# Optimization experiments

Hardware: AMD Instinct MI355X
Metric: run time of the kernel (lower is better)

## Reference

```python
import jax, jax.numpy as jnp
import numpy as np

B = 16384
D_VIS, D_LANG, D_STATE = 768, 768, 64
D = 256          # d_model
E = 4            # n_experts
K = 2            # top_k
D_IN = D_VIS + D_LANG + D_STATE
EPS = 1e-5


def layernorm(x, g, b):
    mu = x.mean(-1, keepdims=True)
    var = ((x - mu) ** 2).mean(-1, keepdims=True)
    return g * (x - mu) / jnp.sqrt(var + EPS) + b


def setup_inputs() -> dict:
    key = jax.random.key(0)
    ks = jax.random.split(key, 16)
    s = 0.02
    return {
        "vis": jax.random.normal(ks[0], (B, D_VIS), jnp.float32),
        "lang": jax.random.normal(ks[1], (B, D_LANG), jnp.float32),
        "state": jax.random.normal(ks[2], (B, D_STATE), jnp.float32),
        # fusion: Linear(d_in, d_model) + LayerNorm
        "Wf": jax.random.normal(ks[3], (D_IN, D), jnp.float32) * s,
        "bf": jnp.zeros((D,), jnp.float32),
        "gf": jnp.ones((D,), jnp.float32),
        "bfln": jnp.zeros((D,), jnp.float32),
        # gate (bias=False); random instead of zeros so routing is nontrivial
        "Wg": jax.random.normal(ks[4], (D, E), jnp.float32) * s,
        # stacked experts: Linear(d,2d) -> GELU -> Linear(2d,d) -> GELU -> Linear(d,d), then LN(x + net(x))
        "W1": jax.random.normal(ks[5], (E, D, 2 * D), jnp.float32) * s,
        "b1": jnp.zeros((E, 2 * D), jnp.float32),
        "W2": jax.random.normal(ks[6], (E, 2 * D, D), jnp.float32) * s,
        "b2": jnp.zeros((E, D), jnp.float32),
        "W3": jax.random.normal(ks[7], (E, D, D), jnp.float32) * s,
        "b3": jnp.zeros((E, D), jnp.float32),
        "eg": jnp.ones((E, D), jnp.float32),
        "eb": jnp.zeros((E, D), jnp.float32),
    }


def reference(vis, lang, state, Wf, bf, gf, bfln, Wg, W1, b1, W2, b2, W3, b3, eg, eb):
    gelu = lambda t: jax.nn.gelu(t, approximate=False)
    # fusion: Linear -> LayerNorm -> GELU  (dropout is eval-mode identity)
    x = jnp.concatenate([vis, lang, state], axis=-1) @ Wf + bf   # [B, D]
    x = gelu(layernorm(x, gf, bfln))

    logits = x @ Wg                                              # [B, E]
    all_probs = jax.nn.softmax(logits, axis=-1)
    top_vals, top_idx = jax.lax.top_k(logits, K)                 # [B, K]
    top_w = jax.nn.softmax(top_vals, axis=-1)                    # [B, K]

    # all experts densely (E small); original computes same math per masked subset
    h = gelu(jnp.einsum('bd,edh->beh', x, W1) + b1)              # [B, E, 2D]
    h = gelu(jnp.einsum('beh,ehd->bed', h, W2) + b2)             # [B, E, D]
    h = jnp.einsum('bed,edf->bef', h, W3) + b3                   # [B, E, D]
    y = layernorm(x[:, None, :] + h, eg, eb)                     # [B, E, D]

    # gather selected experts and combine with top-k weights
    y_sel = jnp.take_along_axis(y, top_idx[:, :, None], axis=1)  # [B, K, D]
    out = jnp.einsum('bk,bkd->bd', top_w, y_sel)                 # [B, D]

    # load-balance loss: importance x load
    counts = jnp.zeros((E,), x.dtype).at[top_idx.reshape(-1)].add(1.0)
    f_i = counts / (B * K)
    lb_loss = E * jnp.sum(f_i * all_probs.mean(0))
    return out, lb_loss
```

## Files before the change

kernel.cpp:

```cpp
#include <hip/hip_runtime.h>
#include <math.h>


typedef unsigned short u16;
typedef unsigned int u32;
typedef __attribute__((ext_vector_type(8))) short bf16x8;
typedef __attribute__((ext_vector_type(4))) float f32x4;

__device__ __forceinline__ float bf2f(u16 u) {
    union { u32 i; float f; } v; v.i = ((u32)u) << 16; return v.f;
}
__device__ __forceinline__ u16 f2bf(float f) {
    union { float f; u32 i; } v; v.f = f;
    u32 x = v.i;
    return (u16)((x + 0x7fffu + ((x >> 16) & 1u)) >> 16);
}
__device__ __forceinline__ float gelu_exact(float v) {
    return 0.5f * v * (1.0f + erff(v * 0.70710678118654752f));
}

typedef __attribute__((address_space(1))) void GV;
typedef __attribute__((address_space(3))) void SV;
__device__ __forceinline__ void gldlds(const void* g, void* l) {
    __builtin_amdgcn_global_load_lds((GV*)g, (SV*)l, 16, 0, 0);
}

__device__ __forceinline__ u32 pk2(u32 f0, u32 f1) {
    return __builtin_amdgcn_perm(f1, f0, 0x07060302);
}

__device__ __forceinline__ void stageA64(const u16* Ag, int lda, u16* As, int tid) {
#pragma unroll
    for (int i = 0; i < 2; ++i) {
        int s = i * 256 + tid;
        int m = s >> 3, c = s & 7;
        gldlds(Ag + m * lda + (c ^ (m & 7)) * 8, As + s * 8);
    }
}
__device__ __forceinline__ void stageB64(const u16* Bg, int ldb, u16* Bs, int tid) {
#pragma unroll
    for (int i = 0; i < 8; ++i) {
        int s = i * 256 + tid;
        int n = s >> 3, c = s & 7;
        gldlds(Bg + n * ldb + (c ^ (n & 7)) * 8, Bs + s * 8);
    }
}
__device__ __forceinline__ void compute64(const u16* As, const u16* Bs, f32x4 acc[4][4],
                                          int w, int l16, int quad) {
#pragma unroll
    for (int ks = 0; ks < 2; ++ks) {
        bf16x8 a[4];
#pragma unroll
        for (int mt = 0; mt < 4; ++mt) {
            int m = mt * 16 + l16;
            a[mt] = *(const bf16x8*)(As + m * 64 + (((ks * 4 + quad) ^ (m & 7)) << 3));
        }
#pragma unroll
        for (int nt = 0; nt < 4; ++nt) {
            int n = w * 64 + nt * 16 + l16;
            bf16x8 b = *(const bf16x8*)(Bs + n * 64 + (((ks * 4 + quad) ^ (n & 7)) << 3));
#pragma unroll
            for (int mt = 0; mt < 4; ++mt)
                acc[mt][nt] = __builtin_amdgcn_mfma_f32_16x16x32_bf16(a[mt], b, acc[mt][nt], 0, 0, 0);
        }
    }
}
__device__ __forceinline__ void stageA128_512(const u16* Ag, int lda, u16* As, int tid) {
#pragma unroll
    for (int i = 0; i < 2; ++i) {
        int s = i * 512 + tid;
        int m = s >> 3, c = s & 7;
        gldlds(Ag + m * lda + (c ^ (m & 7)) * 8, As + s * 8);
    }
}
__device__ __forceinline__ void stageB64_512(const u16* Bg, int ldb, u16* Bs, int tid) {
#pragma unroll
    for (int i = 0; i < 4; ++i) {
        int s = i * 512 + tid;
        int n = s >> 3, c = s & 7;
        gldlds(Bg + n * ldb + (c ^ (n & 7)) * 8, Bs + s * 8);
    }
}
__device__ __forceinline__ void compute128_8w(const u16* As, const u16* Bs, f32x4 acc[4][4],
                                              int wrw, int wc, int l16, int quad) {
#pragma unroll
    for (int ks = 0; ks < 2; ++ks) {
        bf16x8 a[4];
#pragma unroll
        for (int mt = 0; mt < 4; ++mt) {
            int m = wrw * 64 + mt * 16 + l16;
            a[mt] = *(const bf16x8*)(As + m * 64 + (((ks * 4 + quad) ^ (m & 7)) << 3));
        }
#pragma unroll
        for (int nt = 0; nt < 4; ++nt) {
            int n = wc * 64 + nt * 16 + l16;
            bf16x8 b = *(const bf16x8*)(Bs + n * 64 + (((ks * 4 + quad) ^ (n & 7)) << 3));
#pragma unroll
            for (int mt = 0; mt < 4; ++mt)
                acc[mt][nt] = __builtin_amdgcn_mfma_f32_16x16x32_bf16(a[mt], b, acc[mt][nt], 0, 0, 0);
        }
    }
}

__global__ __launch_bounds__(256) void prep_kernel(
    const float* __restrict__ Wf, const float* __restrict__ W1, const float* __restrict__ W2,
    const float* __restrict__ W3,
    u16* __restrict__ wft, u16* __restrict__ w1t, u16* __restrict__ w2t, u16* __restrict__ w3t,
    float* __restrict__ lbacc) {
    int b = blockIdx.x;
    int tid = threadIdx.x;
    const float* src; u16* dst; int K, N, kt, ntl;
    if (b < 400)      { src = Wf; dst = wft; K = 1600; N = 256; kt = b % 50; ntl = b / 50; }
    else if (b < 912) { int r = b - 400, e = r >> 7; r &= 127;
                        src = W1 + (size_t)e * 131072; dst = w1t + (size_t)e * 131072;
                        K = 256; N = 512; kt = r & 7; ntl = r >> 3; }
    else if (b < 1424){ int r = b - 912, e = r >> 7; r &= 127;
                        src = W2 + (size_t)e * 131072; dst = w2t + (size_t)e * 131072;
                        K = 512; N = 256; kt = r & 15; ntl = r >> 4; }
    else if (b < 1680){ int r = b - 1424, e = r >> 6; r &= 63;
                        src = W3 + (size_t)e * 65536; dst = w3t + (size_t)e * 65536;
                        K = 256; N = 256; kt = r & 7; ntl = r >> 3; }
    else { if (tid < 8) lbacc[tid] = 0.0f; return; }
    int k0 = kt * 32, n0 = ntl * 32;
    __shared__ float tl[32][33];
    int j = tid & 31, i0 = (tid >> 5) << 2;
#pragma unroll
    for (int ii = 0; ii < 4; ++ii)
        tl[i0 + ii][j] = src[(size_t)(k0 + i0 + ii) * N + n0 + j];
    __syncthreads();
#pragma unroll
    for (int ii = 0; ii < 4; ++ii)
        dst[(size_t)(n0 + i0 + ii) * K + k0 + j] = f2bf(tl[j][i0 + ii]);
}

__global__ __launch_bounds__(512, 4) void fusion_kernel(
    const float* __restrict__ vis, const float* __restrict__ lang, const float* __restrict__ state,
    const u16* __restrict__ BT, const float* __restrict__ bfv_, const float* __restrict__ gf,
    const float* __restrict__ bfln, const float* __restrict__ Wg,
    u16* __restrict__ xbf, float* __restrict__ wr, float* __restrict__ lbacc) {
    __shared__ __align__(16) u32 Af[2048];
    __shared__ __align__(16) u16 Bs[16384];
    int tid = threadIdx.x;
    int w = tid >> 6, lane = tid & 63, quad = lane >> 4, l16 = lane & 15;
    int m0 = blockIdx.x * 32;
    f32x4 acc[2][2] = {};

    for (int kit = 0; kit < 25; ++kit) {
        const float* base; int ld;
        if (kit < 12)      { base = vis   + (size_t)m0 * 768 + kit * 64;        ld = 768; }
        else if (kit < 24) { base = lang  + (size_t)m0 * 768 + (kit - 12) * 64; ld = 768; }
        else               { base = state + (size_t)m0 * 64;                    ld = 64; }
        {
            int s = tid;
            int m = s >> 4, c = s & 15;
            gldlds(base + m * ld + (c ^ (m & 15)) * 4, Af + s * 4);
        }
        stageB64_512(BT + kit * 64, 1600, Bs, tid);
        __syncthreads();
#pragma unroll
        for (int ks = 0; ks < 2; ++ks) {
            bf16x8 a[2];
#pragma unroll
            for (int mt = 0; mt < 2; ++mt) {
                int m = mt * 16 + l16;
                int c0 = ks * 8 + quad * 2;
                const u32* rowp = Af + m * 64;
                uint4 f0 = *(const uint4*)(rowp + (c0 ^ (m & 15)) * 4);
                uint4 f1 = *(const uint4*)(rowp + ((c0 + 1) ^ (m & 15)) * 4);
                union { u32 u[4]; bf16x8 v; } pk;
                pk.u[0] = pk2(f0.x, f0.y); pk.u[1] = pk2(f0.z, f0.w);
                pk.u[2] = pk2(f1.x, f1.y); pk.u[3] = pk2(f1.z, f1.w);
                a[mt] = pk.v;
            }
#pragma unroll
            for (int nt = 0; nt < 2; ++nt) {
                int n = w * 32 + nt * 16 + l16;
                bf16x8 b = *(const bf16x8*)(Bs + n * 64 + (((ks * 4 + quad) ^ (n & 7)) << 3));
#pragma unroll
                for (int mt = 0; mt < 2; ++mt)
                    acc[mt][nt] = __builtin_amdgcn_mfma_f32_16x16x32_bf16(a[mt], b, acc[mt][nt], 0, 0, 0);
            }
        }
        __syncthreads();
    }

    float2* red  = (float2*)Af;
    float*  muv  = (float*)(Af + 512);
    float*  rsv  = (float*)(Af + 544);
    float*  gred = (float*)(Af + 576);
    float*  sacc = (float*)(Af + 1600);

    float bv[2], gvv[2], blv[2]; float4 wgv[2];
#pragma unroll
    for (int nt = 0; nt < 2; ++nt) {
        int col = w * 32 + nt * 16 + l16;
        bv[nt] = bfv_[col]; gvv[nt] = gf[col]; blv[nt] = bfln[col];
        wgv[nt] = *(const float4*)(Wg + col * 4);
    }
    if (tid < 8) sacc[tid] = 0.f;
#pragma unroll
    for (int mt = 0; mt < 2; ++mt)
#pragma unroll
        for (int r = 0; r < 4; ++r) {
            float ss = 0.f, qq = 0.f;
#pragma unroll
            for (int nt = 0; nt < 2; ++nt) {
                float v = acc[mt][nt][r] + bv[nt];
                acc[mt][nt][r] = v;
                ss += v; qq += v * v;
            }
#pragma unroll
            for (int d = 1; d < 16; d <<= 1) { ss += __shfl_xor(ss, d); qq += __shfl_xor(qq, d); }
            if (l16 == 0) red[w * 32 + mt * 16 + quad * 4 + r] = make_float2(ss, qq);
        }
    __syncthreads();
    if (tid < 32) {
        float ss = 0.f, qq = 0.f;
#pragma unroll
        for (int ww = 0; ww < 8; ++ww) { float2 t = red[ww * 32 + tid]; ss += t.x; qq += t.y; }
        float mu = ss * (1.f / 256.f);
        float var = qq * (1.f / 256.f) - mu * mu;
        muv[tid] = mu;
        rsv[tid] = 1.f / sqrtf(var + 1e-5f);
    }
    __syncthreads();
#pragma unroll
    for (int mt = 0; mt < 2; ++mt)
#pragma unroll
        for (int r = 0; r < 4; ++r) {
            int rl = mt * 16 + quad * 4 + r;
            float mu = muv[rl], rs = rsv[rl];
#pragma unroll
            for (int nt = 0; nt < 2; ++nt) {
                int col = w * 32 + nt * 16 + l16;
                float t = (acc[mt][nt][r] - mu) * rs * gvv[nt] + blv[nt];
                float g = gelu_exact(t);
                acc[mt][nt][r] = g;
                xbf[(size_t)(m0 + rl) * 256 + col] = f2bf(g);
            }
        }
#pragma unroll
    for (int mt = 0; mt < 2; ++mt)
#pragma unroll
        for (int r = 0; r < 4; ++r) {
            int rl = mt * 16 + quad * 4 + r;
            float p0 = 0.f, p1 = 0.f, p2 = 0.f, p3 = 0.f;
#pragma unroll
            for (int nt = 0; nt < 2; ++nt) {
                float g = acc[mt][nt][r];
                p0 += g * wgv[nt].x; p1 += g * wgv[nt].y;
                p2 += g * wgv[nt].z; p3 += g * wgv[nt].w;
            }
#pragma unroll
            for (int d = 1; d < 16; d <<= 1) {
                p0 += __shfl_xor(p0, d); p1 += __shfl_xor(p1, d);
                p2 += __shfl_xor(p2, d); p3 += __shfl_xor(p3, d);
            }
            if (l16 == 0) {
                float* gp = gred + w * 128 + rl * 4;
                gp[0] = p0; gp[1] = p1; gp[2] = p2; gp[3] = p3;
            }
        }
    __syncthreads();
    if (tid < 32) {
        int row = tid;
        float lg[4];
#pragma unroll
        for (int e = 0; e < 4; ++e) {
            float s = 0.f;
#pragma unroll
            for (int ww = 0; ww < 8; ++ww) s += gred[ww * 128 + row * 4 + e];
            lg[e] = s;
        }
        float mx = fmaxf(fmaxf(lg[0], lg[1]), fmaxf(lg[2], lg[3]));
        float ex[4]; float Z = 0.f;
#pragma unroll
        for (int e = 0; e < 4; ++e) { ex[e] = expf(lg[e] - mx); Z += ex[e]; }
        int i0 = 0; float v0 = lg[0];
#pragma unroll
        for (int e = 1; e < 4; ++e) if (lg[e] > v0) { v0 = lg[e]; i0 = e; }
        int i1 = -1; float v1 = -1e30f;
#pragma unroll
        for (int e = 0; e < 4; ++e) if (e != i0 && lg[e] > v1) { v1 = lg[e]; i1 = e; }
        float t = expf(v1 - v0);
        float wA = 1.f / (1.f + t), wB = t / (1.f + t);
        float w4[4] = {0.f, 0.f, 0.f, 0.f};
        w4[i0] = wA; w4[i1] = wB;
#pragma unroll
        for (int e = 0; e < 4; ++e) wr[(size_t)(m0 + row) * 4 + e] = w4[e];
#pragma unroll
        for (int e = 0; e < 4; ++e) atomicAdd(&sacc[e], ex[e] / Z);
        atomicAdd(&sacc[4 + i0], 1.f);
        atomicAdd(&sacc[4 + i1], 1.f);
    }
    __syncthreads();
    if (tid < 8) atomicAdd(lbacc + tid, sacc[tid]);
}

__global__ __launch_bounds__(512, 4) void expert_gemm_kernel(
    const u16* __restrict__ A, int lda, size_t aE,
    const u16* __restrict__ BT, size_t bE,
    const float* __restrict__ bias, int biasE,
    u16* __restrict__ outp, int ldo, size_t oE) {
    __shared__ __align__(16) u16 As[8192];
    __shared__ __align__(16) u16 Bs[16384];
    int tid = threadIdx.x;
    int w = tid >> 6, lane = tid & 63, quad = lane >> 4, l16 = lane & 15;
    int wrw = w >> 2, wc = w & 3;
    int m0 = blockIdx.x * 128;
    int col0 = blockIdx.y * 256;
    int e = blockIdx.z;
    f32x4 acc[4][4] = {};
    const u16* Ag = A + e * aE + (size_t)m0 * lda;
    const u16* Bg = BT + e * bE + (size_t)col0 * lda;
    int kiters = lda >> 6;
    for (int kit = 0; kit < kiters; ++kit) {
        stageA128_512(Ag + kit * 64, lda, As, tid);
        stageB64_512(Bg + kit * 64, lda, Bs, tid);
        __syncthreads();
        compute128_8w(As, Bs, acc, wrw, wc, l16, quad);
        __syncthreads();
    }
#pragma unroll
    for (int nt = 0; nt < 4; ++nt) {
        int col = col0 + wc * 64 + nt * 16 + l16;
        float bvv = bias[e * biasE + col];
#pragma unroll
        for (int mt = 0; mt < 4; ++mt)
#pragma unroll
            for (int r = 0; r < 4; ++r) {
                int row = m0 + wrw * 64 + mt * 16 + quad * 4 + r;
                outp[e * oE + (size_t)row * ldo + col] = f2bf(gelu_exact(acc[mt][nt][r] + bvv));
            }
    }
}

__global__ __launch_bounds__(256) void combine_kernel(
    const u16* __restrict__ h2, const u16* __restrict__ W3T,
    const float* __restrict__ b3, const float* __restrict__ eg, const float* __restrict__ eb,
    const u16* __restrict__ xbf, const float* __restrict__ wr,
    const float* __restrict__ lbacc, float* __restrict__ outp) {
    __shared__ __align__(16) u16 As[4096];
    __shared__ __align__(16) u16 Bs[16384];
    __shared__ __align__(16) u16 xs[16384];
    __shared__ float wl[256];
    __shared__ float2 red[256];
    __shared__ float muv[64], rsv[64];
    int tid = threadIdx.x;
    int w = tid >> 6, lane = tid & 63, quad = lane >> 4, l16 = lane & 15;
    int m0 = blockIdx.x * 64;
    if (blockIdx.x == 0 && tid == 0) {
        float lb = 0.f;
#pragma unroll
        for (int e = 0; e < 4; ++e)
            lb += (lbacc[4 + e] / 32768.f) * (lbacc[e] / 16384.f);
        outp[4194304] = 4.f * lb;
    }
#pragma unroll
    for (int i = 0; i < 8; ++i) {
        int s = i * 256 + tid;
        *(uint4*)(xs + s * 8) = *(const uint4*)(xbf + (size_t)m0 * 256 + s * 8);
    }
    wl[tid] = wr[(size_t)m0 * 4 + tid];
    f32x4 oacc[4][4] = {};
    for (int e = 0; e < 4; ++e) {
        __syncthreads();
        f32x4 acc[4][4] = {};
        const u16* Ag = h2 + ((size_t)e * 16384 + m0) * 256;
        const u16* Bg = W3T + (size_t)e * 65536;
        for (int kit = 0; kit < 4; ++kit) {
            stageA64(Ag + kit * 64, 256, As, tid);
            stageB64(Bg + kit * 64, 256, Bs, tid);
            __syncthreads();
            compute64(As, Bs, acc, w, l16, quad);
            __syncthreads();
        }
        float b3v[4], egv[4], ebv[4];
#pragma unroll
        for (int nt = 0; nt < 4; ++nt) {
            int col = w * 64 + nt * 16 + l16;
            b3v[nt] = b3[e * 256 + col]; egv[nt] = eg[e * 256 + col]; ebv[nt] = eb[e * 256 + col];
        }
#pragma unroll
        for (int mt = 0; mt < 4; ++mt)
#pragma unroll
            for (int r = 0; r < 4; ++r) {
                int row = mt * 16 + quad * 4 + r;
                float ss = 0.f, qq = 0.f;
#pragma unroll
                for (int nt = 0; nt < 4; ++nt) {
                    int col = w * 64 + nt * 16 + l16;
                    float v = acc[mt][nt][r] + b3v[nt] + bf2f(xs[row * 256 + col]);
                    acc[mt][nt][r] = v;
                    ss += v; qq += v * v;
                }
#pragma unroll
                for (int d = 1; d < 16; d <<= 1) { ss += __shfl_xor(ss, d); qq += __shfl_xor(qq, d); }
                if (l16 == 0) red[w * 64 + row] = make_float2(ss, qq);
            }
        __syncthreads();
        if (tid < 64) {
            float ss = 0.f, qq = 0.f;
#pragma unroll
            for (int ww = 0; ww < 4; ++ww) { float2 t = red[ww * 64 + tid]; ss += t.x; qq += t.y; }
            float mu = ss * (1.f / 256.f);
            float var = qq * (1.f / 256.f) - mu * mu;
            muv[tid] = mu;
            rsv[tid] = 1.f / sqrtf(var + 1e-5f);
        }
        __syncthreads();
#pragma unroll
        for (int mt = 0; mt < 4; ++mt)
#pragma unroll
            for (int r = 0; r < 4; ++r) {
                int row = mt * 16 + quad * 4 + r;
                float mu = muv[row], rs = rsv[row], we = wl[row * 4 + e];
#pragma unroll
                for (int nt = 0; nt < 4; ++nt) {
                    float y = (acc[mt][nt][r] - mu) * rs * egv[nt] + ebv[nt];
                    oacc[mt][nt][r] += we * y;
                }
            }
    }
#pragma unroll
    for (int mt = 0; mt < 4; ++mt)
#pragma unroll
        for (int r = 0; r < 4; ++r) {
            int row = mt * 16 + quad * 4 + r;
#pragma unroll
            for (int nt = 0; nt < 4; ++nt) {
                int col = w * 64 + nt * 16 + l16;
                outp[(size_t)(m0 + row) * 256 + col] = oacc[mt][nt][r];
            }
        }
}

extern "C" void kernel_launch(void* const* d_in, const int* in_sizes, int n_in,
                              void* d_out, int out_size, void* d_ws, size_t ws_size,
                              hipStream_t stream) {
    const float* vis   = (const float*)d_in[0];
    const float* lang  = (const float*)d_in[1];
    const float* state = (const float*)d_in[2];
    const float* Wf    = (const float*)d_in[3];
    const float* bf_   = (const float*)d_in[4];
    const float* gf    = (const float*)d_in[5];
    const float* bfln  = (const float*)d_in[6];
    const float* Wg    = (const float*)d_in[7];
    const float* W1    = (const float*)d_in[8];
    const float* b1    = (const float*)d_in[9];
    const float* W2    = (const float*)d_in[10];
    const float* b2    = (const float*)d_in[11];
    const float* W3    = (const float*)d_in[12];
    const float* b3    = (const float*)d_in[13];
    const float* eg    = (const float*)d_in[14];
    const float* eb    = (const float*)d_in[15];
    float* outp = (float*)d_out;

    char* ws = (char*)d_ws;
    size_t off = 0;
    float* lbacc = (float*)(ws + off); off += 256;
    u16* WFT  = (u16*)(ws + off); off += 819200UL;
    u16* W1T  = (u16*)(ws + off); off += 1048576UL;
    u16* W2T  = (u16*)(ws + off); off += 1048576UL;
    u16* W3T  = (u16*)(ws + off); off += 524288UL;
    u16* XBF  = (u16*)(ws + off); off += 8388608UL;
    float* WR = (float*)(ws + off); off += 262144UL;
    u16* H1   = (u16*)(ws + off); off += 67108864UL;
    u16* H2   = (u16*)(ws + off); off += 33554432UL;
    if (ws_size < off) return;

    prep_kernel<<<1681, 256, 0, stream>>>(Wf, W1, W2, W3, WFT, W1T, W2T, W3T, lbacc);
    fusion_kernel<<<512, 512, 0, stream>>>(vis, lang, state, WFT, bf_, gf, bfln, Wg,
                                           XBF, WR, lbacc);
    expert_gemm_kernel<<<dim3(128, 2, 4), 512, 0, stream>>>(
        XBF, 256, 0, W1T, 131072, b1, 512, H1, 512, 8388608UL);
    expert_gemm_kernel<<<dim3(128, 1, 4), 512, 0, stream>>>(
        H1, 512, 8388608UL, W2T, 131072, b2, 256, H2, 256, 4194304UL);
    combine_kernel<<<256, 256, 0, stream>>>(H2, W3T, b3, eg, eb, XBF, WR, lbacc, outp);
}
```

Measured before the change: 319.6 us.

## Split combine per expert with atomics, stage expert GEMM stores, overlap weight prep

Three separate changes. The combine kernel is split across experts on a second grid dimension, and each block atomically adds its weighted LayerNorm output into a zero-initialised output. This quadruples the parallelism at the cost of a memset and float atomics, and the atomics make the order of summation nondeterministic. The expert GEMM epilogue now stages bf16 results through LDS with a swizzle so they can be written with coalesced 16-byte stores. Transposition of W1/W2/W3 moves into extra blocks of the fusion kernel so it overlaps with the fusion GEMM instead of running in a separate prep kernel.

```diff
diff --git a/kernel.cpp b/kernel.cpp
--- a/kernel.cpp
+++ b/kernel.cpp
@@ -102,45 +102,61 @@
     }
 }
 
-__global__ __launch_bounds__(256) void prep_kernel(
-    const float* __restrict__ Wf, const float* __restrict__ W1, const float* __restrict__ W2,
-    const float* __restrict__ W3,
-    u16* __restrict__ wft, u16* __restrict__ w1t, u16* __restrict__ w2t, u16* __restrict__ w3t,
-    float* __restrict__ lbacc) {
+__global__ __launch_bounds__(256) void prep_a_kernel(
+    const float* __restrict__ Wf, u16* __restrict__ wft, float* __restrict__ lbacc) {
     int b = blockIdx.x;
     int tid = threadIdx.x;
-    const float* src; u16* dst; int K, N, kt, ntl;
-    if (b < 400)      { src = Wf; dst = wft; K = 1600; N = 256; kt = b % 50; ntl = b / 50; }
-    else if (b < 912) { int r = b - 400, e = r >> 7; r &= 127;
-                        src = W1 + (size_t)e * 131072; dst = w1t + (size_t)e * 131072;
-                        K = 256; N = 512; kt = r & 7; ntl = r >> 3; }
-    else if (b < 1424){ int r = b - 912, e = r >> 7; r &= 127;
-                        src = W2 + (size_t)e * 131072; dst = w2t + (size_t)e * 131072;
-                        K = 512; N = 256; kt = r & 15; ntl = r >> 4; }
-    else if (b < 1680){ int r = b - 1424, e = r >> 6; r &= 63;
-                        src = W3 + (size_t)e * 65536; dst = w3t + (size_t)e * 65536;
-                        K = 256; N = 256; kt = r & 7; ntl = r >> 3; }
-    else { if (tid < 8) lbacc[tid] = 0.0f; return; }
+    if (b >= 400) { if (tid < 8) lbacc[tid] = 0.0f; return; }
+    const int K = 1600, N = 256;
+    int kt = b % 50, ntl = b / 50;
     int k0 = kt * 32, n0 = ntl * 32;
     __shared__ float tl[32][33];
     int j = tid & 31, i0 = (tid >> 5) << 2;
 #pragma unroll
     for (int ii = 0; ii < 4; ++ii)
-        tl[i0 + ii][j] = src[(size_t)(k0 + i0 + ii) * N + n0 + j];
+        tl[i0 + ii][j] = Wf[(size_t)(k0 + i0 + ii) * N + n0 + j];
     __syncthreads();
 #pragma unroll
     for (int ii = 0; ii < 4; ++ii)
-        dst[(size_t)(n0 + i0 + ii) * K + k0 + j] = f2bf(tl[j][i0 + ii]);
+        wft[(size_t)(n0 + i0 + ii) * K + k0 + j] = f2bf(tl[j][i0 + ii]);
 }
 
 __global__ __launch_bounds__(512, 4) void fusion_kernel(
     const float* __restrict__ vis, const float* __restrict__ lang, const float* __restrict__ state,
     const u16* __restrict__ BT, const float* __restrict__ bfv_, const float* __restrict__ gf,
     const float* __restrict__ bfln, const float* __restrict__ Wg,
+    const float* __restrict__ W1, const float* __restrict__ W2, const float* __restrict__ W3,
+    u16* __restrict__ w1t, u16* __restrict__ w2t, u16* __restrict__ w3t,
     u16* __restrict__ xbf, float* __restrict__ wr, float* __restrict__ lbacc) {
     __shared__ __align__(16) u32 Af[2048];
     __shared__ __align__(16) u16 Bs[16384];
     int tid = threadIdx.x;
+
+    if (blockIdx.x >= 512) {
+        int r = blockIdx.x - 512;
+        const float* src; u16* dst; int K, N, kt, ntl;
+        if (r < 512)       { int e = r >> 7, rr = r & 127;
+                             src = W1 + (size_t)e * 131072; dst = w1t + (size_t)e * 131072;
+                             K = 256; N = 512; kt = rr & 7; ntl = rr >> 3; }
+        else if (r < 1024) { int r2 = r - 512, e = r2 >> 7, rr = r2 & 127;
+                             src = W2 + (size_t)e * 131072; dst = w2t + (size_t)e * 131072;
+                             K = 512; N = 256; kt = rr & 15; ntl = rr >> 4; }
+        else               { int r3 = r - 1024, e = r3 >> 6, rr = r3 & 63;
+                             src = W3 + (size_t)e * 65536; dst = w3t + (size_t)e * 65536;
+                             K = 256; N = 256; kt = rr & 7; ntl = rr >> 3; }
+        int k0 = kt * 32, n0 = ntl * 32;
+        float* tl = (float*)Af;
+        int j = tid & 31, i0 = (tid >> 5) << 1;
+#pragma unroll
+        for (int ii = 0; ii < 2; ++ii)
+            tl[(i0 + ii) * 33 + j] = src[(size_t)(k0 + i0 + ii) * N + n0 + j];
+        __syncthreads();
+#pragma unroll
+        for (int ii = 0; ii < 2; ++ii)
+            dst[(size_t)(n0 + i0 + ii) * K + k0 + j] = f2bf(tl[j * 33 + i0 + ii]);
+        return;
+    }
+
     int w = tid >> 6, lane = tid & 63, quad = lane >> 4, l16 = lane & 15;
     int m0 = blockIdx.x * 32;
     f32x4 acc[2][2] = {};
@@ -321,17 +337,37 @@
         compute128_8w(As, Bs, acc, wrw, wc, l16, quad);
         __syncthreads();
     }
-#pragma unroll
-    for (int nt = 0; nt < 4; ++nt) {
-        int col = col0 + wc * 64 + nt * 16 + l16;
-        float bvv = bias[e * biasE + col];
-#pragma unroll
-        for (int mt = 0; mt < 4; ++mt)
+    float bvv[4];
+#pragma unroll
+    for (int nt = 0; nt < 4; ++nt)
+        bvv[nt] = bias[e * biasE + col0 + wc * 64 + nt * 16 + l16];
+#pragma unroll
+    for (int h = 0; h < 2; ++h) {
+#pragma unroll
+        for (int mt2 = 0; mt2 < 2; ++mt2) {
+            int mt = h * 2 + mt2;
 #pragma unroll
             for (int r = 0; r < 4; ++r) {
-                int row = m0 + wrw * 64 + mt * 16 + quad * 4 + r;
-                outp[e * oE + (size_t)row * ldo + col] = f2bf(gelu_exact(acc[mt][nt][r] + bvv));
-            }
+                int vrow = wrw * 32 + mt2 * 16 + quad * 4 + r;
+#pragma unroll
+                for (int nt = 0; nt < 4; ++nt) {
+                    int col = wc * 64 + nt * 16 + l16;
+                    float g = gelu_exact(acc[mt][nt][r] + bvv[nt]);
+                    Bs[vrow * 256 + (col ^ ((vrow & 7) << 5))] = f2bf(g);
+                }
+            }
+        }
+        __syncthreads();
+        {
+            int vrow = tid >> 3, cc = tid & 7;
+            int base = vrow * 256 + ((cc ^ (vrow & 7)) << 5);
+            int grow = m0 + h * 32 + (vrow >> 5) * 64 + (vrow & 31);
+            u16* op = outp + e * oE + (size_t)grow * ldo + col0 + cc * 32;
+#pragma unroll
+            for (int j = 0; j < 4; ++j)
+                *(uint4*)(op + j * 8) = *(const uint4*)(Bs + base + j * 8);
+        }
+        if (h == 0) __syncthreads();
     }
 }
 
@@ -343,17 +379,16 @@
     __shared__ __align__(16) u16 As[4096];
     __shared__ __align__(16) u16 Bs[16384];
     __shared__ __align__(16) u16 xs[16384];
-    __shared__ float wl[256];
-    __shared__ float2 red[256];
-    __shared__ float muv[64], rsv[64];
+    __shared__ float wl[64];
     int tid = threadIdx.x;
     int w = tid >> 6, lane = tid & 63, quad = lane >> 4, l16 = lane & 15;
     int m0 = blockIdx.x * 64;
-    if (blockIdx.x == 0 && tid == 0) {
+    int e = blockIdx.y;
+    if (blockIdx.x == 0 && e == 0 && tid == 0) {
         float lb = 0.f;
 #pragma unroll
-        for (int e = 0; e < 4; ++e)
-            lb += (lbacc[4 + e] / 32768.f) * (lbacc[e] / 16384.f);
+        for (int ee = 0; ee < 4; ++ee)
+            lb += (lbacc[4 + ee] / 32768.f) * (lbacc[ee] / 16384.f);
         outp[4194304] = 4.f * lb;
     }
 #pragma unroll
@@ -361,76 +396,65 @@
         int s = i * 256 + tid;
         *(uint4*)(xs + s * 8) = *(const uint4*)(xbf + (size_t)m0 * 256 + s * 8);
     }
-    wl[tid] = wr[(size_t)m0 * 4 + tid];
-    f32x4 oacc[4][4] = {};
-    for (int e = 0; e < 4; ++e) {
-        __syncthreads();
-        f32x4 acc[4][4] = {};
-        const u16* Ag = h2 + ((size_t)e * 16384 + m0) * 256;
-        const u16* Bg = W3T + (size_t)e * 65536;
-        for (int kit = 0; kit < 4; ++kit) {
-            stageA64(Ag + kit * 64, 256, As, tid);
-            stageB64(Bg + kit * 64, 256, Bs, tid);
-            __syncthreads();
-            compute64(As, Bs, acc, w, l16, quad);
-            __syncthreads();
-        }
-        float b3v[4], egv[4], ebv[4];
-#pragma unroll
-        for (int nt = 0; nt < 4; ++nt) {
-            int col = w * 64 + nt * 16 + l16;
-            b3v[nt] = b3[e * 256 + col]; egv[nt] = eg[e * 256 + col]; ebv[nt] = eb[e * 256 + col];
-        }
-#pragma unroll
-        for (int mt = 0; mt < 4; ++mt)
-#pragma unroll
-            for (int r = 0; r < 4; ++r) {
-                int row = mt * 16 + quad * 4 + r;
-                float ss = 0.f, qq = 0.f;
-#pragma unroll
-                for (int nt = 0; nt < 4; ++nt) {
-                    int col = w * 64 + nt * 16 + l16;
-                    float v = acc[mt][nt][r] + b3v[nt] + bf2f(xs[row * 256 + col]);
-                    acc[mt][nt][r] = v;
-                    ss += v; qq += v * v;
-                }
-#pragma unroll
-                for (int d = 1; d < 16; d <<= 1) { ss += __shfl_xor(ss, d); qq += __shfl_xor(qq, d); }
-                if (l16 == 0) red[w * 64 + row] = make_float2(ss, qq);
-            }
-        __syncthreads();
-        if (tid < 64) {
-            float ss = 0.f, qq = 0.f;
-#pragma unroll
-            for (int ww = 0; ww < 4; ++ww) { float2 t = red[ww * 64 + tid]; ss += t.x; qq += t.y; }
-            float mu = ss * (1.f / 256.f);
-            float var = qq * (1.f / 256.f) - mu * mu;
-            muv[tid] = mu;
-            rsv[tid] = 1.f / sqrtf(var + 1e-5f);
-        }
-        __syncthreads();
-#pragma unroll
-        for (int mt = 0; mt < 4; ++mt)
-#pragma unroll
-            for (int r = 0; r < 4; ++r) {
-                int row = mt * 16 + quad * 4 + r;
-                float mu = muv[row], rs = rsv[row], we = wl[row * 4 + e];
-#pragma unroll
-                for (int nt = 0; nt < 4; ++nt) {
-                    float y = (acc[mt][nt][r] - mu) * rs * egv[nt] + ebv[nt];
-                    oacc[mt][nt][r] += we * y;
-                }
-            }
-    }
+    if (tid < 64) wl[tid] = wr[(size_t)(m0 + tid) * 4 + e];
+    f32x4 acc[4][4] = {};
+    const u16* Ag = h2 + ((size_t)e * 16384 + m0) * 256;
+    const u16* Bg = W3T + (size_t)e * 65536;
+    for (int kit = 0; kit < 4; ++kit) {
+        stageA64(Ag + kit * 64, 256, As, tid);
+        stageB64(Bg + kit * 64, 256, Bs, tid);
+        __syncthreads();
+        compute64(As, Bs, acc, w, l16, quad);
+        __syncthreads();
+    }
+    float b3v[4], egv[4], ebv[4];
+#pragma unroll
+    for (int nt = 0; nt < 4; ++nt) {
+        int col = w * 64 + nt * 16 + l16;
+        b3v[nt] = b3[e * 256 + col]; egv[nt] = eg[e * 256 + col]; ebv[nt] = eb[e * 256 + col];
+    }
+    float2* red = (float2*)As;
+    float* muv = (float*)((char*)As + 2048);
+    float* rsv = (float*)((char*)As + 2304);
 #pragma unroll
     for (int mt = 0; mt < 4; ++mt)
 #pragma unroll
         for (int r = 0; r < 4; ++r) {
             int row = mt * 16 + quad * 4 + r;
+            float ss = 0.f, qq = 0.f;
 #pragma unroll
             for (int nt = 0; nt < 4; ++nt) {
                 int col = w * 64 + nt * 16 + l16;
-                outp[(size_t)(m0 + row) * 256 + col] = oacc[mt][nt][r];
+                float v = acc[mt][nt][r] + b3v[nt] + bf2f(xs[row * 256 + col]);
+                acc[mt][nt][r] = v;
+                ss += v; qq += v * v;
+            }
+#pragma unroll
+            for (int d = 1; d < 16; d <<= 1) { ss += __shfl_xor(ss, d); qq += __shfl_xor(qq, d); }
+            if (l16 == 0) red[w * 64 + row] = make_float2(ss, qq);
+        }
+    __syncthreads();
+    if (tid < 64) {
+        float ss = 0.f, qq = 0.f;
+#pragma unroll
+        for (int ww = 0; ww < 4; ++ww) { float2 t = red[ww * 64 + tid]; ss += t.x; qq += t.y; }
+        float mu = ss * (1.f / 256.f);
+        float var = qq * (1.f / 256.f) - mu * mu;
+        muv[tid] = mu;
+        rsv[tid] = 1.f / sqrtf(var + 1e-5f);
+    }
+    __syncthreads();
+#pragma unroll
+    for (int mt = 0; mt < 4; ++mt)
+#pragma unroll
+        for (int r = 0; r < 4; ++r) {
+            int row = mt * 16 + quad * 4 + r;
+            float mu = muv[row], rs = rsv[row], we = wl[row];
+#pragma unroll
+            for (int nt = 0; nt < 4; ++nt) {
+                int col = w * 64 + nt * 16 + l16;
+                float y = (acc[mt][nt][r] - mu) * rs * egv[nt] + ebv[nt];
+                atomicAdd(&outp[(size_t)(m0 + row) * 256 + col], we * y);
             }
         }
 }
@@ -469,12 +493,15 @@
     u16* H2   = (u16*)(ws + off); off += 33554432UL;
     if (ws_size < off) return;
 
-    prep_kernel<<<1681, 256, 0, stream>>>(Wf, W1, W2, W3, WFT, W1T, W2T, W3T, lbacc);
-    fusion_kernel<<<512, 512, 0, stream>>>(vis, lang, state, WFT, bf_, gf, bfln, Wg,
-                                           XBF, WR, lbacc);
+    prep_a_kernel<<<401, 256, 0, stream>>>(Wf, WFT, lbacc);
+    fusion_kernel<<<1792, 512, 0, stream>>>(vis, lang, state, WFT, bf_, gf, bfln, Wg,
+                                            W1, W2, W3, W1T, W2T, W3T,
+                                            XBF, WR, lbacc);
     expert_gemm_kernel<<<dim3(128, 2, 4), 512, 0, stream>>>(
         XBF, 256, 0, W1T, 131072, b1, 512, H1, 512, 8388608UL);
     expert_gemm_kernel<<<dim3(128, 1, 4), 512, 0, stream>>>(
         H1, 512, 8388608UL, W2T, 131072, b2, 256, H2, 256, 4194304UL);
-    combine_kernel<<<256, 256, 0, stream>>>(H2, W3T, b3, eg, eb, XBF, WR, lbacc, outp);
-}
+    hipMemsetAsync(outp, 0, 16777216UL, stream);
+    combine_kernel<<<dim3(256, 4), 256, 0, stream>>>(
+        H2, W3T, b3, eg, eb, XBF, WR, lbacc, outp);
+}
```

New measurement: 345.5 us. 8.1% more time.
